# Performance work log

Measured on AMD Instinct MI355X. Metric: run time of the kernel, lower is better.

## Reference

```python
import jax, jax.numpy as jnp
import numpy as np

TEMP = 0.2
M, K, B = 8192, 128, 100


def setup_inputs() -> dict:
    key = jax.random.key(0)
    k1, k2, k3 = jax.random.split(key, 3)
    f = jax.random.normal(k1, (M, K), dtype=jnp.float32)
    features = f / jnp.linalg.norm(f, axis=1, keepdims=True)
    p = jax.random.normal(k2, (B, K), dtype=jnp.float32)
    protos = p / jnp.linalg.norm(p, axis=1, keepdims=True)
    labels = jax.random.randint(k3, (M,), 0, 2 * B, dtype=jnp.int32)
    proto_labels = jnp.arange(B, dtype=jnp.int32)
    return {"features": features, "labels": labels, "protos": protos, "proto_labels": proto_labels}


def reference(features, labels, protos, proto_labels):
    m = features.shape[0]
    dt = features.dtype
    # base = samples whose label appears among prototype labels
    base = (labels[None, :] == proto_labels[:, None]).any(axis=0)  # [M] bool
    novel = ~base
    nf = novel.astype(dt)
    bf = base.astype(dt)

    S = jnp.matmul(features, features.T) / TEMP          # [M, M] sample-sample logits
    P = jnp.matmul(features, protos.T) / TEMP            # [M, B] sample-proto logits

    # novel-novel pair mask: both novel, off-diagonal (fill_diagonal_(0))
    pair = nf[:, None] * nf[None, :] * (1.0 - jnp.eye(m, dtype=dt))  # [M, M]
    expS = jnp.exp(S)

    # --- novel loss (note: original adds RAW ni_pk.sum, not exp -- faithful) ---
    exp_sum = (expS * pair).sum(axis=1)                  # sum_{j novel, j!=i} exp(S_ij)
    denom = exp_sum + P.sum(axis=1)                      # + raw proto logit sum
    safe_den = jnp.where(novel, denom, 1.0)
    cnt = pair.sum(axis=1)                               # novel_label_mask is all-True 1D -> just pair count
    safe_cnt = jnp.where(cnt > 0, cnt, 1.0)
    # sum_j pair_ij * (S_ij - log(den_i)) = (S*pair).sum - log(den)*cnt
    num = (S * pair).sum(axis=1) - jnp.log(safe_den) * cnt
    loss_novel = (-(num / safe_cnt) * nf).sum()

    # --- base loss ---
    safe_lab = jnp.where(base, labels, 0)
    bi_pi = jnp.take_along_axis(P, safe_lab[:, None], axis=1)[:, 0]  # P[i, labels[i]]
    exp_nk = (expS * nf[None, :]).sum(axis=1)            # sum over novel columns
    exp_pk = jnp.exp(P).sum(axis=1)
    loss_base = (-(bi_pi - jnp.log(exp_nk + exp_pk)) * bf).sum()

    return (loss_novel + loss_base) / m
```

## Files before the change

kernel.cpp:

```cpp
#include <hip/hip_runtime.h>
#include <stdint.h>


#define M_TOT 8192
#define K_DIM 128
#define B_PRO 100
#define INV_T 5.0f
#define C_SCALE 7.2134752044448170f
#define LN2    0.6931471805599453f
#define RT    256
#define NT    (M_TOT / RT)
#define NPAIR (NT * (NT - 1) / 2)
#define NBLK  (NT + NPAIR)
#define BS    136
#define PB    112

#if __has_builtin(__builtin_amdgcn_exp2f)
#define EXP2(x) __builtin_amdgcn_exp2f(x)
#else
#define EXP2(x) __expf((x) * 0.6931471805599453f)
#endif

typedef __attribute__((ext_vector_type(8))) short  short8;
typedef __attribute__((ext_vector_type(4))) float  floatx4;

__device__ __forceinline__ unsigned short f2bf(float x) {
    union { float f; unsigned int i; } v; v.f = x;
    return (unsigned short)((v.i + 0x7fffu + ((v.i >> 16) & 1u)) >> 16);
}
__device__ __forceinline__ short8 pack8(float4 a, float4 b) {
    short8 r;
    r[0] = (short)f2bf(a.x); r[1] = (short)f2bf(a.y);
    r[2] = (short)f2bf(a.z); r[3] = (short)f2bf(a.w);
    r[4] = (short)f2bf(b.x); r[5] = (short)f2bf(b.y);
    r[6] = (short)f2bf(b.z); r[7] = (short)f2bf(b.w);
    return r;
}

template<bool DIAG>
__device__ __forceinline__ void sym_body(
        int a, int b, int R0, int C0,
        const float* __restrict__ feat, const int* __restrict__ labels,
        const float* __restrict__ protos, const int* __restrict__ plabels,
        float* __restrict__ rowE, float* __restrict__ rowS,
        int* __restrict__ nfpart, int* __restrict__ nf,
        float* __restrict__ Psum, float* __restrict__ expPsum,
        float* __restrict__ PLab,
        unsigned short* ldsB, float (*colE)[256], float (*colS)[256],
        float* novR, float* novC, int* plabL, int* labRow, float* redD) {
    const int tid = threadIdx.x;
    const int wv = tid >> 6, lane = tid & 63;
    const int quad = lane >> 4, cq = lane & 15;

    if (tid < B_PRO) plabL[tid] = plabels[tid];

    short8 afr[2][4];
    #pragma unroll
    for (int mt = 0; mt < 2; ++mt)
        #pragma unroll
        for (int ks = 0; ks < 4; ++ks) {
            const float* s = feat + (size_t)(R0 + wv * 32 + mt * 16 + cq) * K_DIM
                             + ks * 32 + quad * 8;
            float4 x = ((const float4*)s)[0];
            float4 y = ((const float4*)s)[1];
            afr[mt][ks] = pack8(x, y);
        }
    __syncthreads();

    {
        const int g = (tid < 256) ? (R0 + tid) : (C0 + (tid - 256));
        const int lbl = labels[g];
        int m = 0;
        #pragma unroll 4
        for (int j = 0; j < B_PRO; ++j) m |= (plabL[j] == lbl);
        const float nv = m ? 0.f : 1.f;
        if (tid < 256) { novR[tid] = nv; labRow[tid] = lbl; }
        else novC[tid - 256] = nv;
    }
    __syncthreads();

    float nmR[2][4];
    #pragma unroll
    for (int mt = 0; mt < 2; ++mt)
        #pragma unroll
        for (int r = 0; r < 4; ++r)
            nmR[mt][r] = novR[wv * 32 + mt * 16 + quad * 4 + r];
    float nmcA[16];
    #pragma unroll
    for (int c2 = 0; c2 < 16; ++c2)
        nmcA[c2] = novC[c2 * 16 + cq];

    float accE[2][4], accS[2][4];
    #pragma unroll
    for (int mt = 0; mt < 2; ++mt)
        #pragma unroll
        for (int r = 0; r < 4; ++r) { accE[mt][r] = 0.f; accS[mt][r] = 0.f; }

    const int rbase = R0 + wv * 32 + quad * 4;

    #pragma unroll 1
    for (int half = 0; half < 2; ++half) {
        for (int e = tid; e < 2048; e += 512) {
            const int col = e >> 4, sg = e & 15;
            const float* s = feat + (size_t)(C0 + half * 128 + col) * K_DIM + sg * 8;
            float4 x = ((const float4*)s)[0];
            float4 y = ((const float4*)s)[1];
            ushort4 o0 = make_ushort4(f2bf(x.x*C_SCALE), f2bf(x.y*C_SCALE),
                                      f2bf(x.z*C_SCALE), f2bf(x.w*C_SCALE));
            ushort4 o1 = make_ushort4(f2bf(y.x*C_SCALE), f2bf(y.y*C_SCALE),
                                      f2bf(y.z*C_SCALE), f2bf(y.w*C_SCALE));
            *(ushort4*)&ldsB[col * BS + sg * 8]     = o0;
            *(ushort4*)&ldsB[col * BS + sg * 8 + 4] = o1;
        }
        __syncthreads();

        #pragma unroll 2
        for (int ct8 = 0; ct8 < 8; ++ct8) {
            const int ct = half * 8 + ct8;
            const unsigned short* bp = &ldsB[(ct8 * 16 + cq) * BS + quad * 8];
            short8 b0 = *(const short8*)(bp);
            short8 b1 = *(const short8*)(bp + 32);
            short8 b2 = *(const short8*)(bp + 64);
            short8 b3 = *(const short8*)(bp + 96);

            floatx4 D0 = (floatx4){0.f, 0.f, 0.f, 0.f};
            floatx4 D1 = (floatx4){0.f, 0.f, 0.f, 0.f};
            D0 = __builtin_amdgcn_mfma_f32_16x16x32_bf16(afr[0][0], b0, D0, 0, 0, 0);
            D0 = __builtin_amdgcn_mfma_f32_16x16x32_bf16(afr[0][1], b1, D0, 0, 0, 0);
            D0 = __builtin_amdgcn_mfma_f32_16x16x32_bf16(afr[0][2], b2, D0, 0, 0, 0);
            D0 = __builtin_amdgcn_mfma_f32_16x16x32_bf16(afr[0][3], b3, D0, 0, 0, 0);
            D1 = __builtin_amdgcn_mfma_f32_16x16x32_bf16(afr[1][0], b0, D1, 0, 0, 0);
            D1 = __builtin_amdgcn_mfma_f32_16x16x32_bf16(afr[1][1], b1, D1, 0, 0, 0);
            D1 = __builtin_amdgcn_mfma_f32_16x16x32_bf16(afr[1][2], b2, D1, 0, 0, 0);
            D1 = __builtin_amdgcn_mfma_f32_16x16x32_bf16(afr[1][3], b3, D1, 0, 0, 0);

            const float nmc = nmcA[ct];
            float cpE = 0.f, cpS = 0.f;
            #pragma unroll
            for (int r = 0; r < 4; ++r) {
                float d0 = D0[r], d1 = D1[r];
                float e0 = EXP2(d0), e1 = EXP2(d1);
                if (DIAG) {
                    const int colg = C0 + ct * 16 + cq;
                    const float ex0 = (rbase + r == colg) ? 0.f : 1.f;
                    const float ex1 = (rbase + 16 + r == colg) ? 0.f : 1.f;
                    e0 *= ex0; d0 *= ex0;
                    e1 *= ex1; d1 *= ex1;
                }
                accE[0][r] += e0 * nmc;  cpE += e0 * nmR[0][r];
                accS[0][r] += d0 * nmc;  cpS += d0 * nmR[0][r];
                accE[1][r] += e1 * nmc;  cpE += e1 * nmR[1][r];
                accS[1][r] += d1 * nmc;  cpS += d1 * nmR[1][r];
            }
            cpE += __shfl_xor(cpE, 16); cpE += __shfl_xor(cpE, 32);
            cpS += __shfl_xor(cpS, 16); cpS += __shfl_xor(cpS, 32);
            if (quad == 0) {
                colE[wv][ct * 16 + cq] = cpE;
                colS[wv][ct * 16 + cq] = cpS;
            }
        }
        __syncthreads();
    }

    #pragma unroll
    for (int mt = 0; mt < 2; ++mt)
        #pragma unroll
        for (int r = 0; r < 4; ++r) {
            float e = accE[mt][r], s = accS[mt][r];
            e += __shfl_xor(e, 1); e += __shfl_xor(e, 2);
            e += __shfl_xor(e, 4); e += __shfl_xor(e, 8);
            s += __shfl_xor(s, 1); s += __shfl_xor(s, 2);
            s += __shfl_xor(s, 4); s += __shfl_xor(s, 8);
            accE[mt][r] = e; accS[mt][r] = s;
        }
    if (cq == 0) {
        const size_t slotR = (size_t)b * M_TOT;
        #pragma unroll
        for (int mt = 0; mt < 2; ++mt)
            #pragma unroll
            for (int r = 0; r < 4; ++r) {
                const int rowg = R0 + wv * 32 + mt * 16 + quad * 4 + r;
                rowE[slotR + rowg] = accE[mt][r];
                rowS[slotR + rowg] = accS[mt][r];
            }
    }

    if (!DIAG) {
        if (tid < 256) {
            float ce = 0.f, cs = 0.f;
            #pragma unroll
            for (int w = 0; w < 8; ++w) { ce += colE[w][tid]; cs += colS[w][tid]; }
            const size_t slotC = (size_t)a * M_TOT;
            rowE[slotC + C0 + tid] = ce;
            rowS[slotC + C0 + tid] = cs;
        }
    } else {
        {
            float nvv = (tid < 256) ? novR[tid] : 0.f;
            for (int off = 1; off < 64; off <<= 1) nvv += __shfl_xor(nvv, off);
            if (lane == 0) redD[wv] = nvv;
        }
        if (tid < 256) nf[R0 + tid] = (int)novR[tid];

        for (int idx = tid; idx < 3200; idx += 512) {
            const int pr = idx >> 5, sg = idx & 31;
            float4 v = ((const float4*)protos)[idx];
            *(ushort4*)&ldsB[pr * BS + sg * 4] =
                make_ushort4(f2bf(v.x), f2bf(v.y), f2bf(v.z), f2bf(v.w));
        }
        for (int idx = tid; idx < 384; idx += 512) {
            const int pr = B_PRO + (idx >> 5), sg = idx & 31;
            *(ushort4*)&ldsB[pr * BS + sg * 4] = make_ushort4(0, 0, 0, 0);
        }
        __syncthreads();

        if (tid == 0) {
            float c = 0.f;
            #pragma unroll
            for (int w = 0; w < 8; ++w) c += redD[w];
            nfpart[a] = (int)c;
        }

        float ps2[2][4], es2[2][4], pl2[2][4];
        #pragma unroll
        for (int mt = 0; mt < 2; ++mt)
            #pragma unroll
            for (int r = 0; r < 4; ++r) { ps2[mt][r]=0.f; es2[mt][r]=0.f; pl2[mt][r]=0.f; }

        #pragma unroll 1
        for (int g = 0; g < 7; ++g) {
            const unsigned short* bp = &ldsB[(g * 16 + cq) * BS + quad * 8];
            short8 b0 = *(const short8*)(bp);
            short8 b1 = *(const short8*)(bp + 32);
            short8 b2 = *(const short8*)(bp + 64);
            short8 b3 = *(const short8*)(bp + 96);
            floatx4 E0 = (floatx4){0.f, 0.f, 0.f, 0.f};
            floatx4 E1 = (floatx4){0.f, 0.f, 0.f, 0.f};
            E0 = __builtin_amdgcn_mfma_f32_16x16x32_bf16(afr[0][0], b0, E0, 0, 0, 0);
            E0 = __builtin_amdgcn_mfma_f32_16x16x32_bf16(afr[0][1], b1, E0, 0, 0, 0);
            E0 = __builtin_amdgcn_mfma_f32_16x16x32_bf16(afr[0][2], b2, E0, 0, 0, 0);
            E0 = __builtin_amdgcn_mfma_f32_16x16x32_bf16(afr[0][3], b3, E0, 0, 0, 0);
            E1 = __builtin_amdgcn_mfma_f32_16x16x32_bf16(afr[1][0], b0, E1, 0, 0, 0);
            E1 = __builtin_amdgcn_mfma_f32_16x16x32_bf16(afr[1][1], b1, E1, 0, 0, 0);
            E1 = __builtin_amdgcn_mfma_f32_16x16x32_bf16(afr[1][2], b2, E1, 0, 0, 0);
            E1 = __builtin_amdgcn_mfma_f32_16x16x32_bf16(afr[1][3], b3, E1, 0, 0, 0);
            const int bcol = g * 16 + cq;
            if (bcol < B_PRO) {
                #pragma unroll
                for (int r = 0; r < 4; ++r) {
                    const float Pv0 = E0[r] * INV_T;
                    ps2[0][r] += Pv0; es2[0][r] += __expf(Pv0);
                    if (bcol == labRow[wv * 32 + quad * 4 + r]) pl2[0][r] += Pv0;
                    const float Pv1 = E1[r] * INV_T;
                    ps2[1][r] += Pv1; es2[1][r] += __expf(Pv1);
                    if (bcol == labRow[wv * 32 + 16 + quad * 4 + r]) pl2[1][r] += Pv1;
                }
            }
        }
        #pragma unroll
        for (int mt = 0; mt < 2; ++mt)
            #pragma unroll
            for (int r = 0; r < 4; ++r) {
                float p = ps2[mt][r], e = es2[mt][r], l = pl2[mt][r];
                p += __shfl_xor(p, 1); p += __shfl_xor(p, 2);
                p += __shfl_xor(p, 4); p += __shfl_xor(p, 8);
                e += __shfl_xor(e, 1); e += __shfl_xor(e, 2);
                e += __shfl_xor(e, 4); e += __shfl_xor(e, 8);
                l += __shfl_xor(l, 1); l += __shfl_xor(l, 2);
                l += __shfl_xor(l, 4); l += __shfl_xor(l, 8);
                if (cq == 0) {
                    const int rowg = R0 + wv * 32 + mt * 16 + quad * 4 + r;
                    Psum[rowg] = p; expPsum[rowg] = e; PLab[rowg] = l;
                }
            }
    }
}

__global__ __launch_bounds__(512, 4) void k_sym(
        const float* __restrict__ feat, const int* __restrict__ labels,
        const float* __restrict__ protos, const int* __restrict__ plabels,
        float* __restrict__ rowE, float* __restrict__ rowS,
        int* __restrict__ nfpart, int* __restrict__ nf,
        float* __restrict__ Psum, float* __restrict__ expPsum,
        float* __restrict__ PLab, float* __restrict__ out) {
    __shared__ unsigned short ldsB[128 * BS];
    __shared__ float colE[8][256];
    __shared__ float colS[8][256];
    __shared__ float novR[256];
    __shared__ float novC[256];
    __shared__ int plabL[B_PRO];
    __shared__ int labRow[256];
    __shared__ float redD[8];

    if (blockIdx.x == 0 && threadIdx.x == 0) out[0] = 0.f;

    const int id = blockIdx.x;
    if (id < NT) {
        sym_body<true>(id, id, id * RT, id * RT,
                       feat, labels, protos, plabels, rowE, rowS,
                       nfpart, nf, Psum, expPsum, PLab,
                       ldsB, colE, colS, novR, novC, plabL, labRow, redD);
    } else {
        const int p = id - NT;
        int aa = 0, rem = p;
        while (rem >= NT - 1 - aa) { rem -= (NT - 1 - aa); ++aa; }
        const int bb2 = aa + 1 + rem;
        sym_body<false>(aa, bb2, aa * RT, bb2 * RT,
                        feat, labels, protos, plabels, rowE, rowS,
                        nfpart, nf, Psum, expPsum, PLab,
                        ldsB, colE, colS, novR, novC, plabL, labRow, redD);
    }
}

__global__ __launch_bounds__(128) void k_final(
        const float* __restrict__ rowE, const float* __restrict__ rowS,
        const float* __restrict__ Psum, const float* __restrict__ expPsum,
        const float* __restrict__ PLab, const int* __restrict__ nf,
        const int* __restrict__ nfpart,
        float* __restrict__ out) {
    __shared__ int shNn;
    __shared__ float red[2];
    const int tid = threadIdx.x;
    const int i = blockIdx.x * 128 + tid;

    if (tid < 32) {
        int c = nfpart[tid];
        for (int off = 1; off < 32; off <<= 1) c += __shfl_xor(c, off);
        if (tid == 0) shNn = c;
    }

    float e0 = 0.f, e1 = 0.f, e2 = 0.f, e3 = 0.f;
    float s0 = 0.f, s1 = 0.f, s2 = 0.f, s3 = 0.f;
    #pragma unroll
    for (int s = 0; s < 8; ++s) {
        e0 += rowE[(size_t)(4 * s + 0) * M_TOT + i];
        e1 += rowE[(size_t)(4 * s + 1) * M_TOT + i];
        e2 += rowE[(size_t)(4 * s + 2) * M_TOT + i];
        e3 += rowE[(size_t)(4 * s + 3) * M_TOT + i];
        s0 += rowS[(size_t)(4 * s + 0) * M_TOT + i];
        s1 += rowS[(size_t)(4 * s + 1) * M_TOT + i];
        s2 += rowS[(size_t)(4 * s + 2) * M_TOT + i];
        s3 += rowS[(size_t)(4 * s + 3) * M_TOT + i];
    }
    const float ep = (e0 + e1) + (e2 + e3);
    const float sp = (s0 + s1) + (s2 + s3);

    __syncthreads();
    const int Nn = shNn;
    float contrib;
    if (nf[i]) {
        const float cnt = (float)(Nn - 1);
        const float denom = ep + Psum[i];
        const float num = sp * LN2 - logf(denom) * cnt;
        const float sc = cnt > 0.f ? cnt : 1.f;
        contrib = -(num / sc);
    } else {
        contrib = -(PLab[i] - logf(ep + expPsum[i]));
    }
    for (int off = 1; off < 64; off <<= 1) contrib += __shfl_xor(contrib, off);
    if ((tid & 63) == 0) red[tid >> 6] = contrib;
    __syncthreads();
    if (tid == 0) atomicAdd(out, (red[0] + red[1]) * (1.0f / (float)M_TOT));
}

extern "C" void kernel_launch(void* const* d_in, const int* in_sizes, int n_in,
                              void* d_out, int out_size, void* d_ws, size_t ws_size,
                              hipStream_t stream) {
    const float* feat    = (const float*)d_in[0];
    const int*   labels  = (const int*)d_in[1];
    const float* protos  = (const float*)d_in[2];
    const int*   plabels = (const int*)d_in[3];
    float* out = (float*)d_out;

    char* ws = (char*)d_ws;
    float* rowE    = (float*)ws;
    float* rowS    = (float*)(ws + 1048576);
    int*   nfpart  = (int*)(ws + 2097152);
    int*   nf      = (int*)(ws + 2101248);
    float* Psum    = (float*)(ws + 2134016);
    float* expPsum = (float*)(ws + 2166784);
    float* PLab    = (float*)(ws + 2199552);

    k_sym<<<NBLK, 512, 0, stream>>>(feat, labels, protos, plabels,
                                    rowE, rowS, nfpart, nf,
                                    Psum, expPsum, PLab, out);
    k_final<<<64, 128, 0, stream>>>(rowE, rowS, Psum, expPsum, PLab,
                                    nf, nfpart, out);
}
```

Baseline: 100.0 us.

## Replace per-pair logit sum with linear novel-feature-sum identity

The masked sum of raw logits over novel columns is linear in the features, so it is rewritten as f_i · (sum of novel features) minus the diagonal term. The diagonal blocks accumulate a novel-weighted column sum of the bf16 scaled features, and the final kernel takes a dot product per row. This removes the S accumulation, its shuffles, the colS LDS traffic and the rowS workspace from the hot MFMA loop. It adds a small serial reduction in the diagonal blocks and a per-row 128-wide dot product in k_final, and it changes rounding slightly through the mixed bf16 products.

```diff
diff --git a/kernel.cpp b/kernel.cpp
--- a/kernel.cpp
+++ b/kernel.cpp
@@ -24,6 +24,9 @@
 typedef __attribute__((ext_vector_type(8))) short  short8;
 typedef __attribute__((ext_vector_type(4))) float  floatx4;
 
+__device__ __forceinline__ float bf2f(unsigned short u) {
+    union { unsigned int i; float f; } v; v.i = ((unsigned int)u) << 16; return v.f;
+}
 __device__ __forceinline__ unsigned short f2bf(float x) {
     union { float f; unsigned int i; } v; v.f = x;
     return (unsigned short)((v.i + 0x7fffu + ((v.i >> 16) & 1u)) >> 16);
@@ -42,11 +45,11 @@
         int a, int b, int R0, int C0,
         const float* __restrict__ feat, const int* __restrict__ labels,
         const float* __restrict__ protos, const int* __restrict__ plabels,
-        float* __restrict__ rowE, float* __restrict__ rowS,
+        float* __restrict__ rowE,
         int* __restrict__ nfpart, int* __restrict__ nf,
         float* __restrict__ Psum, float* __restrict__ expPsum,
-        float* __restrict__ PLab,
-        unsigned short* ldsB, float (*colE)[256], float (*colS)[256],
+        float* __restrict__ PLab, float* __restrict__ gpart,
+        unsigned short* ldsB, float (*colE)[256],
         float* novR, float* novC, int* plabL, int* labRow, float* redD) {
     const int tid = threadIdx.x;
     const int wv = tid >> 6, lane = tid & 63;
@@ -90,11 +93,13 @@
     for (int c2 = 0; c2 < 16; ++c2)
         nmcA[c2] = novC[c2 * 16 + cq];
 
-    float accE[2][4], accS[2][4];
+    float accE[2][4];
     #pragma unroll
     for (int mt = 0; mt < 2; ++mt)
         #pragma unroll
-        for (int r = 0; r < 4; ++r) { accE[mt][r] = 0.f; accS[mt][r] = 0.f; }
+        for (int r = 0; r < 4; ++r) accE[mt][r] = 0.f;
+
+    float g_acc = 0.f;
 
     const int rbase = R0 + wv * 32 + quad * 4;
 
@@ -135,29 +140,28 @@
             D1 = __builtin_amdgcn_mfma_f32_16x16x32_bf16(afr[1][3], b3, D1, 0, 0, 0);
 
             const float nmc = nmcA[ct];
-            float cpE = 0.f, cpS = 0.f;
+            float cpE = 0.f;
             #pragma unroll
             for (int r = 0; r < 4; ++r) {
-                float d0 = D0[r], d1 = D1[r];
-                float e0 = EXP2(d0), e1 = EXP2(d1);
+                float e0 = EXP2(D0[r]), e1 = EXP2(D1[r]);
                 if (DIAG) {
                     const int colg = C0 + ct * 16 + cq;
-                    const float ex0 = (rbase + r == colg) ? 0.f : 1.f;
-                    const float ex1 = (rbase + 16 + r == colg) ? 0.f : 1.f;
-                    e0 *= ex0; d0 *= ex0;
-                    e1 *= ex1; d1 *= ex1;
+                    if (rbase + r == colg) e0 = 0.f;
+                    if (rbase + 16 + r == colg) e1 = 0.f;
                 }
                 accE[0][r] += e0 * nmc;  cpE += e0 * nmR[0][r];
-                accS[0][r] += d0 * nmc;  cpS += d0 * nmR[0][r];
                 accE[1][r] += e1 * nmc;  cpE += e1 * nmR[1][r];
-                accS[1][r] += d1 * nmc;  cpS += d1 * nmR[1][r];
             }
             cpE += __shfl_xor(cpE, 16); cpE += __shfl_xor(cpE, 32);
-            cpS += __shfl_xor(cpS, 16); cpS += __shfl_xor(cpS, 32);
-            if (quad == 0) {
-                colE[wv][ct * 16 + cq] = cpE;
-                colS[wv][ct * 16 + cq] = cpS;
-            }
+            if (quad == 0) colE[wv][ct * 16 + cq] = cpE;
+        }
+
+        if (DIAG && tid < 128) {
+            float s = 0.f;
+            #pragma unroll 4
+            for (int c2 = 0; c2 < 128; ++c2)
+                s += novC[half * 128 + c2] * bf2f(ldsB[c2 * BS + tid]);
+            g_acc += s;
         }
         __syncthreads();
     }
@@ -166,12 +170,10 @@
     for (int mt = 0; mt < 2; ++mt)
         #pragma unroll
         for (int r = 0; r < 4; ++r) {
-            float e = accE[mt][r], s = accS[mt][r];
+            float e = accE[mt][r];
             e += __shfl_xor(e, 1); e += __shfl_xor(e, 2);
             e += __shfl_xor(e, 4); e += __shfl_xor(e, 8);
-            s += __shfl_xor(s, 1); s += __shfl_xor(s, 2);
-            s += __shfl_xor(s, 4); s += __shfl_xor(s, 8);
-            accE[mt][r] = e; accS[mt][r] = s;
+            accE[mt][r] = e;
         }
     if (cq == 0) {
         const size_t slotR = (size_t)b * M_TOT;
@@ -181,20 +183,18 @@
             for (int r = 0; r < 4; ++r) {
                 const int rowg = R0 + wv * 32 + mt * 16 + quad * 4 + r;
                 rowE[slotR + rowg] = accE[mt][r];
-                rowS[slotR + rowg] = accS[mt][r];
             }
     }
 
     if (!DIAG) {
         if (tid < 256) {
-            float ce = 0.f, cs = 0.f;
-            #pragma unroll
-            for (int w = 0; w < 8; ++w) { ce += colE[w][tid]; cs += colS[w][tid]; }
-            const size_t slotC = (size_t)a * M_TOT;
-            rowE[slotC + C0 + tid] = ce;
-            rowS[slotC + C0 + tid] = cs;
+            float ce = 0.f;
+            #pragma unroll
+            for (int w = 0; w < 8; ++w) ce += colE[w][tid];
+            rowE[(size_t)a * M_TOT + C0 + tid] = ce;
         }
     } else {
+        if (tid < 128) gpart[a * 128 + tid] = g_acc;
         {
             float nvv = (tid < 256) ? novR[tid] : 0.f;
             for (int off = 1; off < 64; off <<= 1) nvv += __shfl_xor(nvv, off);
@@ -279,13 +279,13 @@
 __global__ __launch_bounds__(512, 4) void k_sym(
         const float* __restrict__ feat, const int* __restrict__ labels,
         const float* __restrict__ protos, const int* __restrict__ plabels,
-        float* __restrict__ rowE, float* __restrict__ rowS,
+        float* __restrict__ rowE,
         int* __restrict__ nfpart, int* __restrict__ nf,
         float* __restrict__ Psum, float* __restrict__ expPsum,
-        float* __restrict__ PLab, float* __restrict__ out) {
+        float* __restrict__ PLab, float* __restrict__ gpart,
+        float* __restrict__ out) {
     __shared__ unsigned short ldsB[128 * BS];
     __shared__ float colE[8][256];
-    __shared__ float colS[8][256];
     __shared__ float novR[256];
     __shared__ float novC[256];
     __shared__ int plabL[B_PRO];
@@ -297,60 +297,79 @@
     const int id = blockIdx.x;
     if (id < NT) {
         sym_body<true>(id, id, id * RT, id * RT,
-                       feat, labels, protos, plabels, rowE, rowS,
-                       nfpart, nf, Psum, expPsum, PLab,
-                       ldsB, colE, colS, novR, novC, plabL, labRow, redD);
+                       feat, labels, protos, plabels, rowE,
+                       nfpart, nf, Psum, expPsum, PLab, gpart,
+                       ldsB, colE, novR, novC, plabL, labRow, redD);
     } else {
         const int p = id - NT;
         int aa = 0, rem = p;
         while (rem >= NT - 1 - aa) { rem -= (NT - 1 - aa); ++aa; }
         const int bb2 = aa + 1 + rem;
         sym_body<false>(aa, bb2, aa * RT, bb2 * RT,
-                        feat, labels, protos, plabels, rowE, rowS,
-                        nfpart, nf, Psum, expPsum, PLab,
-                        ldsB, colE, colS, novR, novC, plabL, labRow, redD);
+                        feat, labels, protos, plabels, rowE,
+                        nfpart, nf, Psum, expPsum, PLab, gpart,
+                        ldsB, colE, novR, novC, plabL, labRow, redD);
     }
 }
 
 __global__ __launch_bounds__(128) void k_final(
-        const float* __restrict__ rowE, const float* __restrict__ rowS,
+        const float* __restrict__ feat,
+        const float* __restrict__ rowE,
         const float* __restrict__ Psum, const float* __restrict__ expPsum,
         const float* __restrict__ PLab, const int* __restrict__ nf,
-        const int* __restrict__ nfpart,
+        const int* __restrict__ nfpart, const float* __restrict__ gpart,
         float* __restrict__ out) {
+    __shared__ float g[128];
     __shared__ int shNn;
     __shared__ float red[2];
     const int tid = threadIdx.x;
     const int i = blockIdx.x * 128 + tid;
 
+    {
+        float s = 0.f;
+        #pragma unroll 4
+        for (int a2 = 0; a2 < 32; ++a2) s += gpart[a2 * 128 + tid];
+        g[tid] = s;
+    }
     if (tid < 32) {
         int c = nfpart[tid];
         for (int off = 1; off < 32; off <<= 1) c += __shfl_xor(c, off);
         if (tid == 0) shNn = c;
     }
+    __syncthreads();
 
     float e0 = 0.f, e1 = 0.f, e2 = 0.f, e3 = 0.f;
-    float s0 = 0.f, s1 = 0.f, s2 = 0.f, s3 = 0.f;
     #pragma unroll
     for (int s = 0; s < 8; ++s) {
         e0 += rowE[(size_t)(4 * s + 0) * M_TOT + i];
         e1 += rowE[(size_t)(4 * s + 1) * M_TOT + i];
         e2 += rowE[(size_t)(4 * s + 2) * M_TOT + i];
         e3 += rowE[(size_t)(4 * s + 3) * M_TOT + i];
-        s0 += rowS[(size_t)(4 * s + 0) * M_TOT + i];
-        s1 += rowS[(size_t)(4 * s + 1) * M_TOT + i];
-        s2 += rowS[(size_t)(4 * s + 2) * M_TOT + i];
-        s3 += rowS[(size_t)(4 * s + 3) * M_TOT + i];
     }
     const float ep = (e0 + e1) + (e2 + e3);
-    const float sp = (s0 + s1) + (s2 + s3);
-
-    __syncthreads();
+
+    const float* fr = feat + (size_t)i * K_DIM;
+    float sZ = 0.f, dd = 0.f;
+    #pragma unroll 8
+    for (int k4 = 0; k4 < 32; ++k4) {
+        float4 v = ((const float4*)fr)[k4];
+        const float fb0 = bf2f(f2bf(v.x)), fc0 = bf2f(f2bf(v.x * C_SCALE));
+        const float fb1 = bf2f(f2bf(v.y)), fc1 = bf2f(f2bf(v.y * C_SCALE));
+        const float fb2 = bf2f(f2bf(v.z)), fc2 = bf2f(f2bf(v.z * C_SCALE));
+        const float fb3 = bf2f(f2bf(v.w)), fc3 = bf2f(f2bf(v.w * C_SCALE));
+        const float* gv = &g[k4 * 4];
+        sZ += fb0 * gv[0]; dd += fb0 * fc0;
+        sZ += fb1 * gv[1]; dd += fb1 * fc1;
+        sZ += fb2 * gv[2]; dd += fb2 * fc2;
+        sZ += fb3 * gv[3]; dd += fb3 * fc3;
+    }
+
     const int Nn = shNn;
     float contrib;
     if (nf[i]) {
         const float cnt = (float)(Nn - 1);
         const float denom = ep + Psum[i];
+        const float sp = sZ - dd;
         const float num = sp * LN2 - logf(denom) * cnt;
         const float sc = cnt > 0.f ? cnt : 1.f;
         contrib = -(num / sc);
@@ -374,16 +393,16 @@
 
     char* ws = (char*)d_ws;
     float* rowE    = (float*)ws;
-    float* rowS    = (float*)(ws + 1048576);
-    int*   nfpart  = (int*)(ws + 2097152);
-    int*   nf      = (int*)(ws + 2101248);
-    float* Psum    = (float*)(ws + 2134016);
-    float* expPsum = (float*)(ws + 2166784);
-    float* PLab    = (float*)(ws + 2199552);
+    int*   nfpart  = (int*)(ws + 1048576);
+    int*   nf      = (int*)(ws + 1052672);
+    float* Psum    = (float*)(ws + 1085440);
+    float* expPsum = (float*)(ws + 1118208);
+    float* PLab    = (float*)(ws + 1150976);
+    float* gpart   = (float*)(ws + 1183744);
 
     k_sym<<<NBLK, 512, 0, stream>>>(feat, labels, protos, plabels,
-                                    rowE, rowS, nfpart, nf,
-                                    Psum, expPsum, PLab, out);
-    k_final<<<64, 128, 0, stream>>>(rowE, rowS, Psum, expPsum, PLab,
-                                    nf, nfpart, out);
-}
+                                    rowE, nfpart, nf,
+                                    Psum, expPsum, PLab, gpart, out);
+    k_final<<<64, 128, 0, stream>>>(feat, rowE, Psum, expPsum, PLab,
+                                    nf, nfpart, gpart, out);
+}
```

Measured after the change: 102.1 us. 2.1% more time.
